# Optimization experiments

Hardware: AMD Instinct MI355X
Metric: run time of the kernel (lower is better)

## Reference

```python
import jax, jax.numpy as jnp
import numpy as np

N, D, O, H, T, S, R, BN = 4096, 256, 256, 256, 512, 8, 4, 2  # nodes, in, out, hidden, text_len, adj_size, relations used, basis_num


def setup_inputs() -> dict:
    key = jax.random.key(0)
    ks = jax.random.split(key, 16)
    sc = 0.05
    return {
        "entity_embeddings": jax.random.normal(ks[0], (N, D), jnp.float32) * sc,
        "text_encodings": jax.random.normal(ks[1], (1, T, 2 * H), jnp.float32) * sc,
        "adj_to_use": jnp.arange(R, dtype=jnp.int32),
        "adj_masks": jax.random.randint(ks[2], (R, N, N), 0, 2, dtype=jnp.int32),
        "text_guids": jax.random.normal(ks[3], (S, 2 * H), jnp.float32) * sc,
        "graph_guids_1": jax.random.normal(ks[4], (S, D), jnp.float32) * sc,
        "graph_guids_2": jax.random.normal(ks[5], (S, D), jnp.float32) * sc,
        "guid_a": jax.random.normal(ks[6], (S,), jnp.float32),
        "basis_V": jax.random.normal(ks[7], (D, BN, O), jnp.float32) * sc,
        "basis_b": jax.random.normal(ks[8], (S, BN), jnp.float32) * sc,
        "W_1": jax.random.normal(ks[9], (2 * H, D), jnp.float32) * sc,
        "W_2": jax.random.normal(ks[10], (2 * H, D), jnp.float32) * sc,
        "ln_gamma": jnp.ones((O,), jnp.float32),
        "ln_beta": jnp.zeros((O,), jnp.float32),
    }


def reference(entity_embeddings, text_encodings, adj_to_use, adj_masks,
              text_guids, graph_guids_1, graph_guids_2, guid_a,
              basis_V, basis_b, W_1, W_2, ln_gamma, ln_beta):
    te = text_encodings[0]                                  # [T, 2H] (batch of 1)
    tg = text_guids[adj_to_use]                             # [R, 2H]
    # text attention: softmax over T, per relation
    att = jax.nn.softmax(te @ tg.T, axis=0)                 # [T, R]
    context = att.T @ te                                    # [R, 2H]
    c1 = context @ W_1                                      # [R, D]
    c2 = context @ W_2
    ga = jax.nn.sigmoid(guid_a[adj_to_use])[:, None]        # [R, 1]
    g1 = ga * graph_guids_1[adj_to_use] + (1.0 - ga) * c1   # [R, D]
    g2 = ga * graph_guids_2[adj_to_use] + (1.0 - ga) * c2
    s1 = entity_embeddings @ g1.T                           # [N, R]
    s2 = entity_embeddings @ g2.T
    # A[r,i,j] = s1[i,r] + s2[j,r], masked softmax over j
    A = s1.T[:, :, None] + s2.T[:, None, :]                 # [R, N, N]
    A = jnp.where(adj_masks == 1, A, jnp.float32(-1e10))
    A = jax.nn.softmax(A, axis=-1)
    fused = jnp.einsum('rij,jd->rid', A, entity_embeddings) # [R, N, D]
    # torch.cat over relations on last dim -> column index r*D + d
    fused_cat = jnp.transpose(fused, (1, 0, 2)).reshape(N, R * D)
    # torch.matmul([R,BN],[D,BN,O]) -> [D,R,O], then .view(R*D, O) (row index d*R + r)
    bb = basis_b[adj_to_use]                                # [R, BN]
    W = jnp.einsum('rb,dbo->dro', bb, basis_V).reshape(D * R, O)
    out = fused_cat @ W                                     # [N, O]
    mu = jnp.mean(out, axis=-1, keepdims=True)
    var = jnp.var(out, axis=-1, keepdims=True)
    out = (out - mu) / jnp.sqrt(var + 1e-5) * ln_gamma + ln_beta
    return jax.nn.relu(out)
```

## Files before the change

kernel.cpp:

```cpp
#include <hip/hip_runtime.h>
#include <hip/hip_bf16.h>


typedef unsigned short u16;
typedef short bf16x8 __attribute__((ext_vector_type(8)));
typedef float f32x4 __attribute__((ext_vector_type(4)));
typedef float f32x8 __attribute__((ext_vector_type(8)));
typedef int   v4i   __attribute__((ext_vector_type(4)));
typedef unsigned int v2u __attribute__((ext_vector_type(2)));

#define G2_OFF    0
#define SC_OFF    4096
#define CTX_OFF   16384
#define WRT_OFF   69632
#define FPT_OFF   593920
#define FUSED_OFF 9506816
#define CAN_OFF   26284032

__device__ __forceinline__ float b2f(u16 u) {
    union { unsigned int i; float f; } v; v.i = ((unsigned int)u) << 16; return v.f;
}
__device__ __forceinline__ u16 f2b(float f) {
    union { float f; unsigned int i; } v; v.f = f;
    return (u16)((v.i + 0x7FFFu + ((v.i >> 16) & 1u)) >> 16);
}
__device__ __forceinline__ float rawf(const void* p, bool isbf, int i) {
    return isbf ? b2f(((const u16*)p)[i]) : ((const float*)p)[i];
}
__device__ __forceinline__ f32x8 raw8(const void* p, bool isbf, int i8) {
    f32x8 o;
    if (isbf) {
        bf16x8 v = *(const bf16x8*)((const u16*)p + i8);
        #pragma unroll
        for (int k = 0; k < 8; ++k) o[k] = b2f((u16)v[k]);
    } else {
        const float* f = (const float*)p + i8;
        float4 a = *(const float4*)f, b = *(const float4*)(f + 4);
        o[0] = a.x; o[1] = a.y; o[2] = a.z; o[3] = a.w;
        o[4] = b.x; o[5] = b.y; o[6] = b.z; o[7] = b.w;
    }
    return o;
}

__global__ __launch_bounds__(512) void k_front(
    const void* __restrict__ ent_raw, const void* __restrict__ te_raw,
    const int* __restrict__ adj, const void* __restrict__ tg_raw,
    const void* __restrict__ bV_raw, const void* __restrict__ bb_raw,
    const unsigned* __restrict__ graw,
    u16* __restrict__ ent_can, float* __restrict__ sc_ws, u16* __restrict__ wrt)
{
    bool isbf = (graw[0] == 0x3F803F80u);
    int b = blockIdx.x, tid = threadIdx.x;
    if (b < 256) {
        int base = b * 4096 + tid;
        if (isbf) {
            const u16* s = (const u16*)ent_raw;
            #pragma unroll
            for (int k = 0; k < 8; ++k) { int i = base + k * 512; ent_can[i] = s[i]; }
        } else {
            const float* s = (const float*)ent_raw;
            #pragma unroll
            for (int k = 0; k < 8; ++k) { int i = base + k * 512; ent_can[i] = f2b(s[i]); }
        }
        return;
    }
    if (b < 384) {
        int b2 = b - 256;
        int r = b2 >> 5, cq = b2 & 31;
        int c = cq * 8 + (tid >> 6);
        int dq = tid & 63;
        int a[4] = {adj[0], adj[1], adj[2], adj[3]};
        #pragma unroll
        for (int dd = 0; dd < 4; ++dd) {
            float w = 0.f;
            #pragma unroll
            for (int bi = 0; bi < 2; ++bi)
                w += rawf(bb_raw, isbf, a[dd] * 2 + bi) *
                     rawf(bV_raw, isbf, ((64 * r + dq) * 2 + bi) * 256 + c);
            wrt[(r * 256 + c) * 256 + dq * 4 + dd] = f2b(w);
        }
        return;
    }
    __shared__ float s_tg[4 * 512];
    int a[4] = {adj[0], adj[1], adj[2], adj[3]};
    for (int idx = tid; idx < 2048; idx += 512) {
        int r = idx >> 9, h = idx & 511;
        s_tg[r * 512 + h] = rawf(tg_raw, isbf, a[r] * 512 + h);
    }
    __syncthreads();
    int b2 = b - 384;
    int t = b2 * 16 + (tid >> 5);
    int h0 = (tid & 31) * 16;
    float s[4] = {0.f, 0.f, 0.f, 0.f};
    #pragma unroll
    for (int half = 0; half < 2; ++half) {
        f32x8 v = raw8(te_raw, isbf, t * 512 + h0 + half * 8);
        #pragma unroll
        for (int k = 0; k < 8; ++k) {
            float tv = v[k]; int h = h0 + half * 8 + k;
            #pragma unroll
            for (int r = 0; r < 4; ++r) s[r] += tv * s_tg[r * 512 + h];
        }
    }
    #pragma unroll
    for (int r = 0; r < 4; ++r) {
        #pragma unroll
        for (int m = 16; m > 0; m >>= 1) s[r] += __shfl_xor(s[r], m);
    }
    if ((tid & 31) == 0) {
        #pragma unroll
        for (int r = 0; r < 4; ++r) sc_ws[t * 4 + r] = s[r];
    }
}

__global__ __launch_bounds__(256) void k_ctx(const void* __restrict__ te_raw,
                                             const float* __restrict__ sc_ws,
                                             const unsigned* __restrict__ graw,
                                             float* __restrict__ ctx_ws) {
    bool isbf = (graw[0] == 0x3F803F80u);
    __shared__ float s_att[512];
    __shared__ float s_red[256];
    __shared__ float s_part[32 * 8];
    int b = blockIdx.x, tid = threadIdx.x;
    int r = b >> 6, hc = b & 63;
    float v0 = sc_ws[tid * 4 + r], v1 = sc_ws[(tid + 256) * 4 + r];
    s_red[tid] = fmaxf(v0, v1);
    __syncthreads();
    for (int st = 128; st > 0; st >>= 1) {
        if (tid < st) s_red[tid] = fmaxf(s_red[tid], s_red[tid + st]);
        __syncthreads();
    }
    float mx = s_red[0];
    __syncthreads();
    float e0 = __expf(v0 - mx), e1 = __expf(v1 - mx);
    s_red[tid] = e0 + e1;
    __syncthreads();
    for (int st = 128; st > 0; st >>= 1) {
        if (tid < st) s_red[tid] += s_red[tid + st];
        __syncthreads();
    }
    float rdn = 1.f / s_red[0];
    __syncthreads();
    s_att[tid] = e0 * rdn;
    s_att[tid + 256] = e1 * rdn;
    __syncthreads();
    int hl = tid & 7, tq = tid >> 3;
    int h = hc * 8 + hl;
    float acc = 0.f;
    #pragma unroll 4
    for (int t = tq * 16; t < tq * 16 + 16; ++t)
        acc += s_att[t] * rawf(te_raw, isbf, t * 512 + h);
    s_part[tq * 8 + hl] = acc;
    __syncthreads();
    if (tid < 8) {
        float c = 0.f;
        #pragma unroll
        for (int s = 0; s < 32; ++s) c += s_part[s * 8 + tid];
        ctx_ws[r * 512 + hc * 8 + tid] = c;
    }
}

__global__ __launch_bounds__(256) void k_g2(const float* __restrict__ ctx_ws,
                                            const int* __restrict__ adj,
                                            const void* __restrict__ W2_raw,
                                            const void* __restrict__ gg2_raw,
                                            const void* __restrict__ ga_raw,
                                            const unsigned* __restrict__ graw,
                                            float* __restrict__ g2ws) {
    bool isbf = (graw[0] == 0x3F803F80u);
    __shared__ float s_ctx[512];
    __shared__ float s_p[2][128];
    int b = blockIdx.x, tid = threadIdx.x;
    int r = b >> 1, dh = b & 1;
    for (int idx = tid; idx < 512; idx += 256) s_ctx[idx] = ctx_ws[r * 512 + idx];
    __syncthreads();
    int dl = tid & 127, th = tid >> 7;
    int d = dh * 128 + dl;
    float acc = 0.f;
    for (int h = th * 256; h < th * 256 + 256; ++h)
        acc += s_ctx[h] * rawf(W2_raw, isbf, h * 256 + d);
    s_p[th][dl] = acc;
    __syncthreads();
    if (th == 0) {
        float tot = s_p[0][dl] + s_p[1][dl];
        int ar = adj[r];
        float gav = 1.f / (1.f + expf(-rawf(ga_raw, isbf, ar)));
        g2ws[r * 256 + d] = gav * rawf(gg2_raw, isbf, ar * 256 + d) + (1.f - gav) * tot;
    }
}

__global__ __launch_bounds__(512) void k_fplus(const u16* __restrict__ entity,
                                               const u16* __restrict__ wrt,
                                               const float* __restrict__ g2ws,
                                               u16* __restrict__ fpt) {
    int b = blockIdx.x, tid = threadIdx.x;
    int r = b & 3, ct = (b >> 2) & 3, jt = b >> 4;
    int c0 = ct * 64, j0 = jt * 256;
    __shared__ __align__(16) u16 lw[64 * 264];
    __shared__ float sg2[256];
    __shared__ float sE[256];
    const u16* wr = wrt + (r * 256 + c0) * 256;
    #pragma unroll
    for (int k = 0; k < 4; ++k) {
        int ci = tid + k * 512; int row = ci >> 5, off = (ci & 31) * 8;
        *(v4i*)(&lw[row * 264 + off]) = *(const v4i*)(wr + row * 256 + off);
    }
    if (tid < 256) sg2[tid] = g2ws[r * 256 + tid];
    __syncthreads();
    int wv = tid >> 6, lane = tid & 63, ln = lane & 15, q = lane >> 4;
    {
        float gl0 = sg2[lane * 4 + 0], gl1 = sg2[lane * 4 + 1];
        float gl2 = sg2[lane * 4 + 2], gl3 = sg2[lane * 4 + 3];
        #pragma unroll 4
        for (int i = 0; i < 32; ++i) {
            int row = j0 + wv * 32 + i;
            v2u e4 = *(const v2u*)(entity + row * 256 + lane * 4);
            float s = b2f((u16)(e4.x & 0xFFFFu)) * gl0
                    + b2f((u16)(e4.x >> 16))     * gl1
                    + b2f((u16)(e4.y & 0xFFFFu)) * gl2
                    + b2f((u16)(e4.y >> 16))     * gl3;
            #pragma unroll
            for (int m = 32; m > 0; m >>= 1) s += __shfl_xor(s, m);
            if (lane == 0) sE[wv * 32 + i] = expf(s);
        }
    }
    __syncthreads();
    f32x4 acc[4][2] = {};
    for (int ks = 0; ks < 8; ++ks) {
        bf16x8 afr[4], bfr[2];
        #pragma unroll
        for (int mt = 0; mt < 4; ++mt)
            afr[mt] = *(const bf16x8*)(&lw[(mt * 16 + ln) * 264 + ks * 32 + q * 8]);
        #pragma unroll
        for (int nt = 0; nt < 2; ++nt) {
            int j = j0 + (wv * 2 + nt) * 16 + ln;
            bfr[nt] = *(const bf16x8*)(entity + j * 256 + ks * 32 + q * 8);
        }
        #pragma unroll
        for (int mt = 0; mt < 4; ++mt)
            #pragma unroll
            for (int nt = 0; nt < 2; ++nt)
                acc[mt][nt] = __builtin_amdgcn_mfma_f32_16x16x32_bf16(afr[mt], bfr[nt], acc[mt][nt], 0, 0, 0);
    }
    #pragma unroll
    for (int nt = 0; nt < 2; ++nt) {
        int jl = (wv * 2 + nt) * 16 + ln;
        int j = j0 + jl;
        float e2j = sE[jl];
        int kt = j >> 5, kk = j & 31;
        u16* dst = fpt + (((size_t)(r * 128 + kt)) * 272 << 5);
        #pragma unroll
        for (int mt = 0; mt < 4; ++mt)
            #pragma unroll
            for (int reg = 0; reg < 4; ++reg) {
                int c = c0 + mt * 16 + q * 4 + reg;
                dst[(c << 5) + kk] = f2b(acc[mt][nt][reg] * e2j);
            }
    }
    if (ct == 0) {
        #pragma unroll
        for (int s = 0; s < 8; ++s) {
            int l = s * 512 + tid;
            int kk = l & 31, cl = (l >> 5) & 15, ktl = l >> 9;
            int kt = jt * 8 + ktl;
            fpt[(((size_t)(r * 128 + kt) * 272 + 256 + cl) << 5) + kk] =
                (cl == 0) ? f2b(sE[ktl * 32 + kk]) : (u16)0;
        }
    }
}

__global__ __launch_bounds__(512) void k_big(const int* __restrict__ masks,
                                             const u16* __restrict__ fpt,
                                             float* __restrict__ fused) {
    __shared__ __align__(16) u16 lm[2][64 * 40];
    __shared__ __align__(16) u16 lf[2][272 * 40];
    __shared__ float lden[64];
    int b = blockIdx.x, tid = threadIdx.x;
    int xcd = b & 7; int r = xcd & 3;
    int it = (b >> 3) + ((xcd >> 2) << 5);
    long i0 = (long)it * 64;
    const int* mbase = masks + ((long)r << 24) + i0 * 4096;
    const u16* fbase = fpt + (size_t)r * 128 * 272 * 32;
    int mrow = tid >> 3, mch = tid & 7;
    int wave = tid >> 6, lane = tid & 63, ln = lane & 15, q = lane >> 4;
    int mg = wave >> 2, ng = wave & 3;

    f32x4 acc[2][4] = {};
    f32x4 accD0 = {}, accD1 = {};

    struct Slot { v4i pm, f0, f1, f2; };
    Slot s0, s1, s2, s3;
    auto load_slot = [&](int kt, Slot& s) {
        s.pm = __builtin_nontemporal_load((const v4i*)(mbase + mrow * 4096 + kt * 32 + mch * 4));
        const u16* su = fbase + (size_t)kt * 8704;
        s.f0 = *(const v4i*)(su + tid * 8);
        s.f1 = *(const v4i*)(su + (tid + 512) * 8);
        if (tid < 64) s.f2 = *(const v4i*)(su + (tid + 1024) * 8);
    };
    auto stage = [&](int par, const Slot& s) {
        {
            unsigned m0 = (unsigned)s.pm.x * 0x3F80u, m1 = (unsigned)s.pm.y * 0x3F80u;
            unsigned m2 = (unsigned)s.pm.z * 0x3F80u, m3 = (unsigned)s.pm.w * 0x3F80u;
            v2u w; w.x = m0 | (m1 << 16); w.y = m2 | (m3 << 16);
            *(v2u*)(&lm[par][mrow * 40 + mch * 4]) = w;
        }
        u16* dst = &lf[par][0];
        *(v4i*)(dst + (tid >> 2) * 40 + (tid & 3) * 8) = s.f0;
        { int ci = tid + 512; *(v4i*)(dst + (ci >> 2) * 40 + (ci & 3) * 8) = s.f1; }
        if (tid < 64) { int ci = tid + 1024; *(v4i*)(dst + (ci >> 2) * 40 + (ci & 3) * 8) = s.f2; }
    };
    auto step = [&](int k, Slot& sM, Slot& sF) {
        const u16* msrc = &lm[k & 1][0];
        const u16* src  = &lf[k & 1][0];
        bf16x8 a0 = *(const bf16x8*)(msrc + (mg * 32 + ln) * 40 + q * 8);
        bf16x8 a1 = *(const bf16x8*)(msrc + (mg * 32 + 16 + ln) * 40 + q * 8);
        if (k + 1 < 128) stage((k + 1) & 1, sF);
        if (k + 4 < 128) load_slot(k + 4, sM);
        #pragma unroll
        for (int nt = 0; nt < 4; ++nt) {
            bf16x8 bf = *(const bf16x8*)(src + ((ng * 4 + nt) * 16 + ln) * 40 + q * 8);
            acc[0][nt] = __builtin_amdgcn_mfma_f32_16x16x32_bf16(a0, bf, acc[0][nt], 0, 0, 0);
            acc[1][nt] = __builtin_amdgcn_mfma_f32_16x16x32_bf16(a1, bf, acc[1][nt], 0, 0, 0);
        }
        if (ng == 3) {
            bf16x8 bf = *(const bf16x8*)(src + (256 + ln) * 40 + q * 8);
            accD0 = __builtin_amdgcn_mfma_f32_16x16x32_bf16(a0, bf, accD0, 0, 0, 0);
            accD1 = __builtin_amdgcn_mfma_f32_16x16x32_bf16(a1, bf, accD1, 0, 0, 0);
        }
        __syncthreads();
    };

    load_slot(0, s0);
    load_slot(1, s1);
    load_slot(2, s2);
    load_slot(3, s3);
    stage(0, s0);
    __syncthreads();
    #pragma unroll 1
    for (int kt = 0; kt < 128; kt += 4) {
        step(kt,     s0, s1);
        step(kt + 1, s1, s2);
        step(kt + 2, s2, s3);
        step(kt + 3, s3, s0);
    }

    if (ng == 3 && ln == 0) {
        #pragma unroll
        for (int reg = 0; reg < 4; ++reg) {
            lden[mg * 32 + q * 4 + reg]      = accD0[reg];
            lden[mg * 32 + 16 + q * 4 + reg] = accD1[reg];
        }
    }
    __syncthreads();
    float* fb = fused + ((long)r * 4096 + i0) * 256;
    #pragma unroll
    for (int mt = 0; mt < 2; ++mt) {
        float rd[4];
        #pragma unroll
        for (int reg = 0; reg < 4; ++reg) rd[reg] = 1.0f / lden[mg * 32 + mt * 16 + q * 4 + reg];
        #pragma unroll
        for (int nt = 0; nt < 4; ++nt) {
            int c = (ng * 4 + nt) * 16 + ln;
            #pragma unroll
            for (int reg = 0; reg < 4; ++reg) {
                int row = mg * 32 + mt * 16 + q * 4 + reg;
                __builtin_nontemporal_store(acc[mt][nt][reg] * rd[reg], fb + row * 256 + c);
            }
        }
    }
}

__global__ __launch_bounds__(256) void k_ln(const float* __restrict__ fused,
                                            const void* __restrict__ gamma_raw,
                                            const void* __restrict__ beta_raw,
                                            const unsigned* __restrict__ graw,
                                            void* __restrict__ outraw) {
    __shared__ float part[8];
    int i = blockIdx.x, o = threadIdx.x;
    bool isbf = (graw[0] == 0x3F803F80u);
    float x = 0.f;
    for (int r = 0; r < 4; ++r)
        x += __builtin_nontemporal_load(fused + ((long)(r << 12) + i) * 256 + o);
    float s = x;
    #pragma unroll
    for (int st = 32; st > 0; st >>= 1) s += __shfl_xor(s, st);
    int w = o >> 6;
    if ((o & 63) == 0) part[w] = s;
    __syncthreads();
    float mu = (part[0] + part[1] + part[2] + part[3]) * (1.f / 256.f);
    float v = x - mu;
    float qv = v * v;
    #pragma unroll
    for (int st = 32; st > 0; st >>= 1) qv += __shfl_xor(qv, st);
    if ((o & 63) == 0) part[4 + w] = qv;
    __syncthreads();
    float var = (part[4] + part[5] + part[6] + part[7]) * (1.f / 256.f);
    float y = v * rsqrtf(var + 1e-5f) * rawf(gamma_raw, isbf, o) + rawf(beta_raw, isbf, o);
    float res = fmaxf(y, 0.f);
    if (isbf) ((u16*)outraw)[i * 256 + o] = f2b(res);
    else      ((float*)outraw)[i * 256 + o] = res;
}

extern "C" void kernel_launch(void* const* d_in, const int* in_sizes, int n_in,
                              void* d_out, int out_size, void* d_ws, size_t ws_size,
                              hipStream_t stream) {
    const int* adj   = (const int*)d_in[2];
    const int* masks = (const int*)d_in[3];
    const unsigned* graw = (const unsigned*)d_in[12];
    char* ws = (char*)d_ws;
    float* g2ws = (float*)(ws + G2_OFF);
    float* scws = (float*)(ws + SC_OFF);
    float* ctxw = (float*)(ws + CTX_OFF);
    u16*   wrt  = (u16*)(ws + WRT_OFF);
    u16*   fpt  = (u16*)(ws + FPT_OFF);
    float* fus  = (float*)(ws + FUSED_OFF);
    u16*   ent  = (u16*)(ws + CAN_OFF);

    k_front<<<416, 512, 0, stream>>>(d_in[0], d_in[1], adj, d_in[4],
                                     d_in[8], d_in[9], graw, ent, scws, wrt);
    k_ctx<<<256, 256, 0, stream>>>(d_in[1], scws, graw, ctxw);
    k_g2<<<8, 256, 0, stream>>>(ctxw, adj, d_in[11], d_in[6], d_in[7], graw, g2ws);
    k_fplus<<<256, 512, 0, stream>>>(ent, wrt, g2ws, fpt);
    k_big<<<256, 512, 0, stream>>>(masks, fpt, fus);
    k_ln<<<4096, 256, 0, stream>>>(fus, d_in[12], d_in[13], graw, d_out);
}
```

Measured before the change: 489.0 us.

## Halve k_big row tile to 32 rows, double grid, swizzle LDS instead of padding

The main masked-softmax aggregation kernel now processes 32 rows per block instead of 64, launching 512 blocks rather than 256 so every CU on the device gets work and more blocks can be resident. LDS tiles drop their 40-element row padding in favour of an XOR swizzle on 32-element rows, which cuts shared memory per block while still avoiding bank conflicts. The cost is that each block now loads the same per-relation feature tiles for half as many rows, which doubles feature-tile traffic per output row. Each wave also issues half as many MFMAs per shared-memory load.

Measured after the change: 497.7 us. Within noise of the previous version (+1.8%).

```diff
diff --git a/kernel.cpp b/kernel.cpp
--- a/kernel.cpp
+++ b/kernel.cpp
@@ -269,63 +269,68 @@
     }
 }
 
-__global__ __launch_bounds__(512) void k_big(const int* __restrict__ masks,
-                                             const u16* __restrict__ fpt,
-                                             float* __restrict__ fused) {
-    __shared__ __align__(16) u16 lm[2][64 * 40];
-    __shared__ __align__(16) u16 lf[2][272 * 40];
-    __shared__ float lden[64];
+__global__ __launch_bounds__(512, 4) void k_big(const int* __restrict__ masks,
+                                                const u16* __restrict__ fpt,
+                                                float* __restrict__ fused) {
+    __shared__ __align__(16) u16 lm[2][32 * 32];
+    __shared__ __align__(16) u16 lf[2][272 * 32];
+    __shared__ float lden[32];
     int b = blockIdx.x, tid = threadIdx.x;
     int xcd = b & 7; int r = xcd & 3;
-    int it = (b >> 3) + ((xcd >> 2) << 5);
-    long i0 = (long)it * 64;
+    int it = (b >> 3) + ((xcd >> 2) << 6);
+    long i0 = (long)it * 32;
     const int* mbase = masks + ((long)r << 24) + i0 * 4096;
     const u16* fbase = fpt + (size_t)r * 128 * 272 * 32;
-    int mrow = tid >> 3, mch = tid & 7;
     int wave = tid >> 6, lane = tid & 63, ln = lane & 15, q = lane >> 4;
     int mg = wave >> 2, ng = wave & 3;
-
-    f32x4 acc[2][4] = {};
-    f32x4 accD0 = {}, accD1 = {};
+    int swb = (ln >> 1) & 3;
+    int rq = (q ^ swb) * 8;
+    int srowF = tid >> 2, schF = tid & 3;
+    int sswF = (schF ^ ((srowF >> 1) & 3)) * 8;
+    int srowM = tid >> 3, schM = tid & 7;
+    int sswM = ((schM >> 1) ^ ((srowM >> 1) & 3)) * 8 + (schM & 1) * 4;
+
+    f32x4 acc[4] = {};
+    f32x4 accD = {};
 
     struct Slot { v4i pm, f0, f1, f2; };
     Slot s0, s1, s2, s3;
     auto load_slot = [&](int kt, Slot& s) {
-        s.pm = __builtin_nontemporal_load((const v4i*)(mbase + mrow * 4096 + kt * 32 + mch * 4));
         const u16* su = fbase + (size_t)kt * 8704;
         s.f0 = *(const v4i*)(su + tid * 8);
         s.f1 = *(const v4i*)(su + (tid + 512) * 8);
         if (tid < 64) s.f2 = *(const v4i*)(su + (tid + 1024) * 8);
+        if (tid < 256) {
+            const int* mp = mbase + srowM * 4096 + kt * 32 + schM * 4;
+            s.pm = __builtin_nontemporal_load((const v4i*)mp);
+        }
     };
     auto stage = [&](int par, const Slot& s) {
-        {
+        u16* dst = &lf[par][0];
+        *(v4i*)(dst + srowF * 32 + sswF) = s.f0;
+        *(v4i*)(dst + (128 + srowF) * 32 + sswF) = s.f1;
+        if (tid < 64) *(v4i*)(dst + (256 + srowF) * 32 + sswF) = s.f2;
+        if (tid < 256) {
             unsigned m0 = (unsigned)s.pm.x * 0x3F80u, m1 = (unsigned)s.pm.y * 0x3F80u;
             unsigned m2 = (unsigned)s.pm.z * 0x3F80u, m3 = (unsigned)s.pm.w * 0x3F80u;
             v2u w; w.x = m0 | (m1 << 16); w.y = m2 | (m3 << 16);
-            *(v2u*)(&lm[par][mrow * 40 + mch * 4]) = w;
-        }
-        u16* dst = &lf[par][0];
-        *(v4i*)(dst + (tid >> 2) * 40 + (tid & 3) * 8) = s.f0;
-        { int ci = tid + 512; *(v4i*)(dst + (ci >> 2) * 40 + (ci & 3) * 8) = s.f1; }
-        if (tid < 64) { int ci = tid + 1024; *(v4i*)(dst + (ci >> 2) * 40 + (ci & 3) * 8) = s.f2; }
+            *(v2u*)(&lm[par][srowM * 32 + sswM]) = w;
+        }
     };
     auto step = [&](int k, Slot& sM, Slot& sF) {
         const u16* msrc = &lm[k & 1][0];
         const u16* src  = &lf[k & 1][0];
-        bf16x8 a0 = *(const bf16x8*)(msrc + (mg * 32 + ln) * 40 + q * 8);
-        bf16x8 a1 = *(const bf16x8*)(msrc + (mg * 32 + 16 + ln) * 40 + q * 8);
+        bf16x8 a0 = *(const bf16x8*)(msrc + (mg * 16 + ln) * 32 + rq);
         if (k + 1 < 128) stage((k + 1) & 1, sF);
         if (k + 4 < 128) load_slot(k + 4, sM);
         #pragma unroll
         for (int nt = 0; nt < 4; ++nt) {
-            bf16x8 bf = *(const bf16x8*)(src + ((ng * 4 + nt) * 16 + ln) * 40 + q * 8);
-            acc[0][nt] = __builtin_amdgcn_mfma_f32_16x16x32_bf16(a0, bf, acc[0][nt], 0, 0, 0);
-            acc[1][nt] = __builtin_amdgcn_mfma_f32_16x16x32_bf16(a1, bf, acc[1][nt], 0, 0, 0);
+            bf16x8 bf = *(const bf16x8*)(src + ((ng * 4 + nt) * 16 + ln) * 32 + rq);
+            acc[nt] = __builtin_amdgcn_mfma_f32_16x16x32_bf16(a0, bf, acc[nt], 0, 0, 0);
         }
         if (ng == 3) {
-            bf16x8 bf = *(const bf16x8*)(src + (256 + ln) * 40 + q * 8);
-            accD0 = __builtin_amdgcn_mfma_f32_16x16x32_bf16(a0, bf, accD0, 0, 0, 0);
-            accD1 = __builtin_amdgcn_mfma_f32_16x16x32_bf16(a1, bf, accD1, 0, 0, 0);
+            bf16x8 bf = *(const bf16x8*)(src + (256 + ln) * 32 + rq);
+            accD = __builtin_amdgcn_mfma_f32_16x16x32_bf16(a0, bf, accD, 0, 0, 0);
         }
         __syncthreads();
     };
@@ -346,26 +351,21 @@
 
     if (ng == 3 && ln == 0) {
         #pragma unroll
+        for (int reg = 0; reg < 4; ++reg)
+            lden[mg * 16 + q * 4 + reg] = accD[reg];
+    }
+    __syncthreads();
+    float* fb = fused + ((long)r * 4096 + i0) * 256;
+    float rd[4];
+    #pragma unroll
+    for (int reg = 0; reg < 4; ++reg) rd[reg] = 1.0f / lden[mg * 16 + q * 4 + reg];
+    #pragma unroll
+    for (int nt = 0; nt < 4; ++nt) {
+        int c = (ng * 4 + nt) * 16 + ln;
+        #pragma unroll
         for (int reg = 0; reg < 4; ++reg) {
-            lden[mg * 32 + q * 4 + reg]      = accD0[reg];
-            lden[mg * 32 + 16 + q * 4 + reg] = accD1[reg];
-        }
-    }
-    __syncthreads();
-    float* fb = fused + ((long)r * 4096 + i0) * 256;
-    #pragma unroll
-    for (int mt = 0; mt < 2; ++mt) {
-        float rd[4];
-        #pragma unroll
-        for (int reg = 0; reg < 4; ++reg) rd[reg] = 1.0f / lden[mg * 32 + mt * 16 + q * 4 + reg];
-        #pragma unroll
-        for (int nt = 0; nt < 4; ++nt) {
-            int c = (ng * 4 + nt) * 16 + ln;
-            #pragma unroll
-            for (int reg = 0; reg < 4; ++reg) {
-                int row = mg * 32 + mt * 16 + q * 4 + reg;
-                __builtin_nontemporal_store(acc[mt][nt][reg] * rd[reg], fb + row * 256 + c);
-            }
+            int row = mg * 16 + q * 4 + reg;
+            __builtin_nontemporal_store(acc[nt][reg] * rd[reg], fb + row * 256 + c);
         }
     }
 }
@@ -421,6 +421,6 @@
     k_ctx<<<256, 256, 0, stream>>>(d_in[1], scws, graw, ctxw);
     k_g2<<<8, 256, 0, stream>>>(ctxw, adj, d_in[11], d_in[6], d_in[7], graw, g2ws);
     k_fplus<<<256, 512, 0, stream>>>(ent, wrt, g2ws, fpt);
-    k_big<<<256, 512, 0, stream>>>(masks, fpt, fus);
+    k_big<<<512, 512, 0, stream>>>(masks, fpt, fus);
     k_ln<<<4096, 256, 0, stream>>>(fus, d_in[12], d_in[13], graw, d_out);
 }
```
